# Optimization experiments

Measured on AMD Instinct MI355X. Metric: run time of the kernel, lower is better.

The kernel has to match this reference:

```python
import jax, jax.numpy as jnp
import numpy as np
from jax import lax

COMMITMENT_COST = 0.25

def setup_inputs() -> dict:
    key = jax.random.key(0)
    k1, k2, k3 = jax.random.split(key, 3)
    B, T, D, Q, K = 32, 8192, 8, 8, 1024
    return {
        "x": jax.random.normal(k1, (B, T, D), dtype=jnp.float32),
        "codebooks": jax.random.normal(k2, (Q, K, D), dtype=jnp.float32),
        "post_scale": jnp.ones((Q,), dtype=jnp.float32),
        "post_bias": jnp.zeros((Q,), dtype=jnp.float32),
        "conv_w": jax.random.normal(k3, (D, D), dtype=jnp.float32),
        "conv_b": jnp.zeros((D,), dtype=jnp.float32),
    }

def reference(x, codebooks, post_scale, post_bias, conv_w, conv_b):
    # Residual VQ with STE fix (use_ste_fix=True, use_cosine_sim=False).
    # x: [B, T, D]; codebooks: [Q, K, D]
    def step(carry, params):
        residual, qsum, loss = carry
        cb, s, b = params  # cb: [K, D]
        # squared L2 distances [B, T, K] = |r|^2 + |c|^2 - 2 r.c
        d2 = ((residual ** 2).sum(-1, keepdims=True)
              + (cb ** 2).sum(-1)
              - 2.0 * jnp.einsum('btd,kd->btk', residual, cb))
        idx = jnp.argmin(d2, axis=-1)          # [B, T]
        embeds = cb[idx]                        # gather [B, T, D]
        # straight-through estimator
        embeds_st = residual + lax.stop_gradient(embeds - residual)
        qsum = qsum + embeds_st * s + b
        new_res = residual - embeds
        loss = loss + jnp.mean((lax.stop_gradient(new_res) - embeds) ** 2)
        return (new_res, qsum, loss), idx

    init = (x, jnp.zeros_like(x), jnp.float32(0.0))
    (_, qsum, loss), codes = lax.scan(step, init, (codebooks, post_scale, post_bias))
    # final_conv: 1x1 Conv1d over channels == dense over last dim
    quantized = jnp.einsum('btd,ed->bte', qsum, conv_w) + conv_b
    return quantized, loss * COMMITMENT_COST, codes  # codes: [Q, B, T]
```

## Files before the change

kernel.cpp:

```cpp
#include <hip/hip_runtime.h>
#include <math.h>

constexpr int Bq = 32;
constexpr int Tq = 8192;
constexpr int Dq = 8;
constexpr int Qq = 8;
constexpr int Kq = 1024;
constexpr int NTOK = Bq * Tq;
constexpr float LOSS_SCALE = 0.25f / (float)(Bq * Tq * Dq);

constexpr int WS_QSTRIDE = 9216;
constexpr int WS_CNMAX   = 8 * WS_QSTRIDE;
constexpr size_t WS_NEED_BYTES = (size_t)(WS_CNMAX + 8) * 4;

typedef __attribute__((ext_vector_type(8))) short short8;
typedef __attribute__((ext_vector_type(4))) float f32x4;
typedef __attribute__((ext_vector_type(4))) unsigned int u32x4;


__device__ __forceinline__ void gload_lds16(const void* gsrc, void* ldst) {
    __builtin_amdgcn_global_load_lds(
        (const __attribute__((address_space(1))) unsigned int*)gsrc,
        (__attribute__((address_space(3))) unsigned int*)ldst,
        16, 0, 0);
}

__global__ __launch_bounds__(512)
void rvq_prep(const float* __restrict__ codebooks, float* __restrict__ ws)
{
    __shared__ float s_red[8];
    const int tid  = threadIdx.x;
    const int lane = tid & 63;
    const int wave = tid >> 6;
    const int q    = blockIdx.x;
    const float* cbq = codebooks + (size_t)q * Kq * Dq;
    float* wq = ws + (size_t)q * WS_QSTRIDE;
    unsigned* frag = reinterpret_cast<unsigned*>(wq);
    float* cnh = wq + Kq * 8;

    float nmax = 0.0f;
#pragma unroll
    for (int it = 0; it < 2; ++it) {
        int n = tid + it * 512;
        const float4* cp = reinterpret_cast<const float4*>(cbq + (size_t)n * 8);
        float4 ca = cp[0], cc = cp[1];
        float c[8] = {ca.x, ca.y, ca.z, ca.w, cc.x, cc.y, cc.z, cc.w};
        float nn = __fmul_rn(c[0], c[0]);
#pragma unroll
        for (int d = 1; d < 8; ++d)
            nn = __fadd_rn(nn, __fmul_rn(c[d], c[d]));
        cnh[n] = -0.5f * nn;
        nmax = fmaxf(nmax, nn);
        unsigned hb[8], lb[8];
#pragma unroll
        for (int d = 0; d < 8; ++d) {
            union { float f; unsigned u; } v; v.f = c[d];
            hb[d] = (v.u + 0x7FFFu + ((v.u >> 16) & 1u)) >> 16;
            union { unsigned u; float f; } h; h.u = hb[d] << 16;
            union { float f; unsigned u; } w; w.f = __fsub_rn(c[d], h.f);
            lb[d] = (w.u + 0x7FFFu + ((w.u >> 16) & 1u)) >> 16;
        }
        u32x4 wh = {hb[0] | (hb[1] << 16), hb[2] | (hb[3] << 16),
                    hb[4] | (hb[5] << 16), hb[6] | (hb[7] << 16)};
        u32x4 wl = {lb[0] | (lb[1] << 16), lb[2] | (lb[3] << 16),
                    lb[4] | (lb[5] << 16), lb[6] | (lb[7] << 16)};
        reinterpret_cast<u32x4*>(frag)[n * 2]     = wh;
        reinterpret_cast<u32x4*>(frag)[n * 2 + 1] = wl;
    }
#pragma unroll
    for (int off = 32; off >= 1; off >>= 1)
        nmax = fmaxf(nmax, __shfl_xor(nmax, off, 64));
    if (lane == 0) s_red[wave] = nmax;
    __syncthreads();
    if (tid == 0) {
        float m = s_red[0];
#pragma unroll
        for (int i = 1; i < 8; ++i) m = fmaxf(m, s_red[i]);
        ws[WS_CNMAX + q] = m;
    }
}

__global__ __launch_bounds__(512, 4)
void rvq_main(const float* __restrict__ x,
              const float* __restrict__ codebooks,
              const float* __restrict__ post_scale,
              const float* __restrict__ post_bias,
              const float* __restrict__ conv_w,
              const float* __restrict__ conv_b,
              const float* __restrict__ ws,
              float* __restrict__ out)
{
    __shared__ __align__(16) unsigned s_all[Kq * 8 + Kq];
    unsigned* s_frag = s_all;
    float* s_cnh = reinterpret_cast<float*>(s_all + Kq * 8);

    const int tid  = threadIdx.x;
    const int lane = tid & 63;
    const int wave = tid >> 6;
    const int quad = lane >> 4;
    const int col  = lane & 15;
    const int wbase = blockIdx.x * 256 + wave * 32;

    float rg[2][Dq];
#pragma unroll
    for (int g = 0; g < 2; ++g) {
        const float4* xp = reinterpret_cast<const float4*>(
            x + (size_t)(wbase + g * 16 + col) * Dq);
        float4 a = xp[0], b = xp[1];
        rg[g][0]=a.x; rg[g][1]=a.y; rg[g][2]=a.z; rg[g][3]=a.w;
        rg[g][4]=b.x; rg[g][5]=b.y; rg[g][6]=b.z; rg[g][7]=b.w;
    }

    float qso[Dq];
#pragma unroll
    for (int d = 0; d < Dq; ++d) qso[d] = 0.0f;
    float lossacc = 0.0f;

    float* out_quant = out;
    float* out_loss  = out + (size_t)NTOK * Dq;
    float* out_codes = out_loss + 1;
    const float* ws_cnmax = ws + WS_CNMAX;

    for (int q = 0; q < Qq; ++q) {
        const float* cbq = codebooks + (size_t)q * Kq * Dq;
        const float* wq = ws + (size_t)q * WS_QSTRIDE;

        {
            const char* src_base = reinterpret_cast<const char*>(wq);
            char* dst_base = reinterpret_cast<char*>(s_all);
            const int l16 = lane * 16;
#pragma unroll
            for (int c = 0; c < 4; ++c) {
                const int off = (wave * 4 + c) * 1024;
                gload_lds16(src_base + off + l16, dst_base + off);
            }
            if (wave < 4) {
                const int off = 32768 + wave * 1024;
                gload_lds16(src_base + off + l16, dst_base + off);
            }
        }
        const float cnmax = ws_cnmax[q];
        __syncthreads();

        float rn_own[2];
        short8 bfrag[2];
#pragma unroll
        for (int g = 0; g < 2; ++g) {
            float n = __fmul_rn(rg[g][0], rg[g][0]);
#pragma unroll
            for (int d = 1; d < 8; ++d)
                n = __fadd_rn(n, __fmul_rn(rg[g][d], rg[g][d]));
            rn_own[g] = n;
            short8 bf;
#pragma unroll
            for (int d = 0; d < 8; ++d) {
                union { float f; unsigned u; } v; v.f = rg[g][d];
                unsigned hbb = (v.u + 0x7FFFu + ((v.u >> 16) & 1u)) >> 16;
                union { unsigned u; float f; } h; h.u = hbb << 16;
                union { float f; unsigned u; } w; w.f = __fsub_rn(rg[g][d], h.f);
                unsigned lbb = (w.u + 0x7FFFu + ((w.u >> 16) & 1u)) >> 16;
                bf[d] = (short)((quad >> 1) ? lbb : hbb);
            }
            bfrag[g] = bf;
        }

        float m1[2]  = {-__builtin_inff(), -__builtin_inff()};
        float m2g[2] = {-__builtin_inff(), -__builtin_inff()};
        int   gtile[2] = {0, 0};
        const int fsel = (quad & 1) * 4;
        const int quad4 = quad * 4;
#pragma unroll 2
        for (int tile = 0; tile < Kq / 16; ++tile) {
            f32x4 cinit = *reinterpret_cast<const f32x4*>(s_cnh + tile * 16 + quad4);
            int fb = (tile * 16 + col) * 8 + fsel;
            uint2 w0 = *reinterpret_cast<const uint2*>(s_frag + fb);
            uint2 w1 = *reinterpret_cast<const uint2*>(s_frag + fb + 2);
            u32x4 wa = {w0.x, w0.y, w1.x, w1.y};
            short8 afrag = __builtin_bit_cast(short8, wa);
#pragma unroll
            for (int g = 0; g < 2; ++g) {
                f32x4 acc = __builtin_amdgcn_mfma_f32_16x16x32_bf16(afrag, bfrag[g], cinit, 0, 0, 0);
                float t = fmaxf(fmaxf(fmaxf(acc[0], acc[1]), acc[2]), acc[3]);
                bool gt = t > m1[g];
                gtile[g] = gt ? tile : gtile[g];
                m2g[g] = fmaxf(m2g[g], fminf(m1[g], t));
                m1[g]  = fmaxf(m1[g], t);
            }
        }

        float M1[2], M2[2];
        int bk[2], fl[2];
#pragma unroll
        for (int g = 0; g < 2; ++g) {
            int base = gtile[g] * 16 + quad4;
            float best = -__builtin_inff(), sec = -__builtin_inff();
            int breg = 0;
#pragma unroll
            for (int r = 0; r < 4; ++r) {
                int k = base + r;
                const float4* cp = reinterpret_cast<const float4*>(cbq + (size_t)k * 8);
                float4 ca = cp[0], cc = cp[1];
                float dot = __fmul_rn(rg[g][0], ca.x);
                dot = fmaf(rg[g][1], ca.y, dot);
                dot = fmaf(rg[g][2], ca.z, dot);
                dot = fmaf(rg[g][3], ca.w, dot);
                dot = fmaf(rg[g][4], cc.x, dot);
                dot = fmaf(rg[g][5], cc.y, dot);
                dot = fmaf(rg[g][6], cc.z, dot);
                dot = fmaf(rg[g][7], cc.w, dot);
                float Dx = __fadd_rn(dot, s_cnh[k]);
                bool w = Dx > best;
                sec = fmaxf(sec, fminf(best, Dx));
                breg = w ? r : breg;
                best = fmaxf(best, Dx);
            }
            M1[g] = best;
            M2[g] = fmaxf(sec, m2g[g]);
            bk[g] = base + breg;
        }

#pragma unroll
        for (int g = 0; g < 2; ++g) {
            float A1 = M1[g], A2 = M2[g]; int K1 = bk[g];
#pragma unroll
            for (int m = 16; m <= 32; m <<= 1) {
                float o1 = __shfl_xor(A1, m, 64);
                float o2 = __shfl_xor(A2, m, 64);
                int   ok = __shfl_xor(K1, m, 64);
                bool ow = (o1 > A1) || (o1 == A1 && ok < K1);
                A2 = ow ? fmaxf(A1, o2) : fmaxf(o1, A2);
                A1 = ow ? o1 : A1; K1 = ow ? ok : K1;
            }
            float margin = (rn_own[g] + cnmax) * 6e-5f;
            fl[g] = (__fsub_rn(A1, A2) <= margin) ? 1 : 0;
            bk[g] = K1;
        }

#pragma unroll
        for (int g = 0; g < 2; ++g) {
            unsigned long long msk = __ballot(fl[g] && (quad == g));
            while (msk) {
                int p = __builtin_ctzll(msk); msk &= (msk - 1);
                float rt[8];
#pragma unroll
                for (int d = 0; d < 8; ++d) rt[d] = __shfl(rg[g][d], p, 64);
                float rnt = __shfl(rn_own[g], p, 64);
                float bb = __builtin_inff(); int bkk = 0;
#pragma unroll 2
                for (int i = 0; i < 16; ++i) {
                    int k = lane + 64 * i;
                    const float4* cp = reinterpret_cast<const float4*>(cbq + (size_t)k * 8);
                    float4 ca = cp[0], cc = cp[1];
                    float c8[8] = {ca.x, ca.y, ca.z, ca.w, cc.x, cc.y, cc.z, cc.w};
                    float cn = __fmul_rn(c8[0], c8[0]);
#pragma unroll
                    for (int d = 1; d < 8; ++d)
                        cn = __fadd_rn(cn, __fmul_rn(c8[d], c8[d]));
                    float dot = __fmul_rn(rt[0], c8[0]);
                    dot = fmaf(rt[1], c8[1], dot);
                    dot = fmaf(rt[2], c8[2], dot);
                    dot = fmaf(rt[3], c8[3], dot);
                    dot = fmaf(rt[4], c8[4], dot);
                    dot = fmaf(rt[5], c8[5], dot);
                    dot = fmaf(rt[6], c8[6], dot);
                    dot = fmaf(rt[7], c8[7], dot);
                    float d2 = fmaf(dot, -2.0f, __fadd_rn(rnt, cn));
                    if (d2 < bb) { bb = d2; bkk = k; }
                }
#pragma unroll
                for (int mm = 1; mm <= 32; mm <<= 1) {
                    float ob = __shfl_xor(bb, mm, 64);
                    int   ok = __shfl_xor(bkk, mm, 64);
                    if (ob < bb || (ob == bb && ok < bkk)) { bb = ob; bkk = ok; }
                }
                if (col == (p & 15)) bk[g] = bkk;
            }
        }

        const float sc = post_scale[q];
        const float bi = post_bias[q];
#pragma unroll
        for (int g = 0; g < 2; ++g) {
            if (quad == g)
                out_codes[(size_t)q * NTOK + wbase + g * 16 + col] = (float)bk[g];
            const float4* ep = reinterpret_cast<const float4*>(cbq + (size_t)bk[g] * 8);
            float4 ea = ep[0], eb = ep[1];
            float e[8] = {ea.x, ea.y, ea.z, ea.w, eb.x, eb.y, eb.z, eb.w};
#pragma unroll
            for (int d = 0; d < 8; ++d) {
                float rd = rg[g][d];
                float est = __fadd_rn(rd, __fsub_rn(e[d], rd));
                if (quad == g) {
                    qso[d] = __fadd_rn(__fadd_rn(qso[d], __fmul_rn(est, sc)), bi);
                }
                float nr = __fsub_rn(rd, e[d]);
                float df = __fsub_rn(nr, e[d]);
                if (quad == g) lossacc = fmaf(df, df, lossacc);
                rg[g][d] = nr;
            }
        }
        __syncthreads();
    }

    if (quad < 2) {
        float o[8];
#pragma unroll
        for (int e2 = 0; e2 < 8; ++e2) {
            float acc = __fmul_rn(qso[0], conv_w[e2 * 8 + 0]);
#pragma unroll
            for (int d = 1; d < 8; ++d)
                acc = fmaf(qso[d], conv_w[e2 * 8 + d], acc);
            o[e2] = __fadd_rn(acc, conv_b[e2]);
        }
        float4* op = reinterpret_cast<float4*>(
            out_quant + (size_t)(wbase + quad * 16 + col) * Dq);
        op[0] = make_float4(o[0], o[1], o[2], o[3]);
        op[1] = make_float4(o[4], o[5], o[6], o[7]);
    }

    float v = lossacc;
#pragma unroll
    for (int off = 32; off >= 1; off >>= 1)
        v += __shfl_xor(v, off, 64);
    if (lane == 0)
        atomicAdd(out_loss, v * LOSS_SCALE);
}

__global__ __launch_bounds__(512, 2)
void rvq_mono(const float* __restrict__ x,
              const float* __restrict__ codebooks,
              const float* __restrict__ post_scale,
              const float* __restrict__ post_bias,
              const float* __restrict__ conv_w,
              const float* __restrict__ conv_b,
              float* __restrict__ out)
{
    __shared__ __align__(16) unsigned s_frag[Kq * 8];
    __shared__ __align__(16) float s_cnh[Kq];
    __shared__ float s_red[8];

    const int tid  = threadIdx.x;
    const int lane = tid & 63;
    const int wave = tid >> 6;
    const int quad = lane >> 4;
    const int col  = lane & 15;
    const int wbase = blockIdx.x * 256 + wave * 32;

    float rg[2][Dq];
#pragma unroll
    for (int g = 0; g < 2; ++g) {
        const float4* xp = reinterpret_cast<const float4*>(
            x + (size_t)(wbase + g * 16 + col) * Dq);
        float4 a = xp[0], b = xp[1];
        rg[g][0]=a.x; rg[g][1]=a.y; rg[g][2]=a.z; rg[g][3]=a.w;
        rg[g][4]=b.x; rg[g][5]=b.y; rg[g][6]=b.z; rg[g][7]=b.w;
    }

    float qso[Dq];
#pragma unroll
    for (int d = 0; d < Dq; ++d) qso[d] = 0.0f;
    float lossacc = 0.0f;

    float* out_quant = out;
    float* out_loss  = out + (size_t)NTOK * Dq;
    float* out_codes = out_loss + 1;

    for (int q = 0; q < Qq; ++q) {
        const float* cbq = codebooks + (size_t)q * Kq * Dq;

        float nmax = 0.0f;
#pragma unroll
        for (int it = 0; it < 2; ++it) {
            int n = tid + it * 512;
            const float4* cp = reinterpret_cast<const float4*>(cbq + (size_t)n * 8);
            float4 ca = cp[0], cc = cp[1];
            float c[8] = {ca.x, ca.y, ca.z, ca.w, cc.x, cc.y, cc.z, cc.w};
            float nn = __fmul_rn(c[0], c[0]);
#pragma unroll
            for (int d = 1; d < 8; ++d)
                nn = __fadd_rn(nn, __fmul_rn(c[d], c[d]));
            s_cnh[n] = -0.5f * nn;
            nmax = fmaxf(nmax, nn);
            unsigned hb[8], lb[8];
#pragma unroll
            for (int d = 0; d < 8; ++d) {
                union { float f; unsigned u; } v; v.f = c[d];
                hb[d] = (v.u + 0x7FFFu + ((v.u >> 16) & 1u)) >> 16;
                union { unsigned u; float f; } h; h.u = hb[d] << 16;
                union { float f; unsigned u; } w; w.f = __fsub_rn(c[d], h.f);
                lb[d] = (w.u + 0x7FFFu + ((w.u >> 16) & 1u)) >> 16;
            }
            u32x4 wh = {hb[0] | (hb[1] << 16), hb[2] | (hb[3] << 16),
                        hb[4] | (hb[5] << 16), hb[6] | (hb[7] << 16)};
            u32x4 wl = {lb[0] | (lb[1] << 16), lb[2] | (lb[3] << 16),
                        lb[4] | (lb[5] << 16), lb[6] | (lb[7] << 16)};
            reinterpret_cast<u32x4*>(s_frag)[n * 2]     = wh;
            reinterpret_cast<u32x4*>(s_frag)[n * 2 + 1] = wl;
        }
#pragma unroll
        for (int off = 32; off >= 1; off >>= 1)
            nmax = fmaxf(nmax, __shfl_xor(nmax, off, 64));
        if (lane == 0) s_red[wave] = nmax;
        __syncthreads();
        float cnmax = s_red[0];
#pragma unroll
        for (int i = 1; i < 8; ++i) cnmax = fmaxf(cnmax, s_red[i]);

        float rn_own[2];
        short8 bfrag[2];
#pragma unroll
        for (int g = 0; g < 2; ++g) {
            float n = __fmul_rn(rg[g][0], rg[g][0]);
#pragma unroll
            for (int d = 1; d < 8; ++d)
                n = __fadd_rn(n, __fmul_rn(rg[g][d], rg[g][d]));
            rn_own[g] = n;
            short8 bf;
#pragma unroll
            for (int d = 0; d < 8; ++d) {
                union { float f; unsigned u; } v; v.f = rg[g][d];
                unsigned hbb = (v.u + 0x7FFFu + ((v.u >> 16) & 1u)) >> 16;
                union { unsigned u; float f; } h; h.u = hbb << 16;
                union { float f; unsigned u; } w; w.f = __fsub_rn(rg[g][d], h.f);
                unsigned lbb = (w.u + 0x7FFFu + ((w.u >> 16) & 1u)) >> 16;
                bf[d] = (short)((quad >> 1) ? lbb : hbb);
            }
            bfrag[g] = bf;
        }

        float m1[2]  = {-__builtin_inff(), -__builtin_inff()};
        float m2g[2] = {-__builtin_inff(), -__builtin_inff()};
        int   gtile[2] = {0, 0};
        const int fsel = (quad & 1) * 4;
        const int quad4 = quad * 4;
#pragma unroll 2
        for (int tile = 0; tile < Kq / 16; ++tile) {
            f32x4 cinit = *reinterpret_cast<const f32x4*>(s_cnh + tile * 16 + quad4);
            int fb = (tile * 16 + col) * 8 + fsel;
            uint2 w0 = *reinterpret_cast<const uint2*>(s_frag + fb);
            uint2 w1 = *reinterpret_cast<const uint2*>(s_frag + fb + 2);
            u32x4 wa = {w0.x, w0.y, w1.x, w1.y};
            short8 afrag = __builtin_bit_cast(short8, wa);
#pragma unroll
            for (int g = 0; g < 2; ++g) {
                f32x4 acc = __builtin_amdgcn_mfma_f32_16x16x32_bf16(afrag, bfrag[g], cinit, 0, 0, 0);
                float t = fmaxf(fmaxf(fmaxf(acc[0], acc[1]), acc[2]), acc[3]);
                bool gt = t > m1[g];
                gtile[g] = gt ? tile : gtile[g];
                m2g[g] = fmaxf(m2g[g], fminf(m1[g], t));
                m1[g]  = fmaxf(m1[g], t);
            }
        }

        float M1[2], M2[2];
        int bk[2], fl[2];
#pragma unroll
        for (int g = 0; g < 2; ++g) {
            int base = gtile[g] * 16 + quad4;
            float best = -__builtin_inff(), sec = -__builtin_inff();
            int breg = 0;
#pragma unroll
            for (int r = 0; r < 4; ++r) {
                int k = base + r;
                const float4* cp = reinterpret_cast<const float4*>(cbq + (size_t)k * 8);
                float4 ca = cp[0], cc = cp[1];
                float dot = __fmul_rn(rg[g][0], ca.x);
                dot = fmaf(rg[g][1], ca.y, dot);
                dot = fmaf(rg[g][2], ca.z, dot);
                dot = fmaf(rg[g][3], ca.w, dot);
                dot = fmaf(rg[g][4], cc.x, dot);
                dot = fmaf(rg[g][5], cc.y, dot);
                dot = fmaf(rg[g][6], cc.z, dot);
                dot = fmaf(rg[g][7], cc.w, dot);
                float Dx = __fadd_rn(dot, s_cnh[k]);
                bool w = Dx > best;
                sec = fmaxf(sec, fminf(best, Dx));
                breg = w ? r : breg;
                best = fmaxf(best, Dx);
            }
            M1[g] = best;
            M2[g] = fmaxf(sec, m2g[g]);
            bk[g] = base + breg;
        }

#pragma unroll
        for (int g = 0; g < 2; ++g) {
            float A1 = M1[g], A2 = M2[g]; int K1 = bk[g];
#pragma unroll
            for (int m = 16; m <= 32; m <<= 1) {
                float o1 = __shfl_xor(A1, m, 64);
                float o2 = __shfl_xor(A2, m, 64);
                int   ok = __shfl_xor(K1, m, 64);
                bool ow = (o1 > A1) || (o1 == A1 && ok < K1);
                A2 = ow ? fmaxf(A1, o2) : fmaxf(o1, A2);
                A1 = ow ? o1 : A1; K1 = ow ? ok : K1;
            }
            float margin = (rn_own[g] + cnmax) * 6e-5f;
            fl[g] = (__fsub_rn(A1, A2) <= margin) ? 1 : 0;
            bk[g] = K1;
        }

#pragma unroll
        for (int g = 0; g < 2; ++g) {
            unsigned long long msk = __ballot(fl[g] && (quad == g));
            while (msk) {
                int p = __builtin_ctzll(msk); msk &= (msk - 1);
                float rt[8];
#pragma unroll
                for (int d = 0; d < 8; ++d) rt[d] = __shfl(rg[g][d], p, 64);
                float rnt = __shfl(rn_own[g], p, 64);
                float bb = __builtin_inff(); int bkk = 0;
#pragma unroll 2
                for (int i = 0; i < 16; ++i) {
                    int k = lane + 64 * i;
                    const float4* cp = reinterpret_cast<const float4*>(cbq + (size_t)k * 8);
                    float4 ca = cp[0], cc = cp[1];
                    float c8[8] = {ca.x, ca.y, ca.z, ca.w, cc.x, cc.y, cc.z, cc.w};
                    float cn = __fmul_rn(c8[0], c8[0]);
#pragma unroll
                    for (int d = 1; d < 8; ++d)
                        cn = __fadd_rn(cn, __fmul_rn(c8[d], c8[d]));
                    float dot = __fmul_rn(rt[0], c8[0]);
                    dot = fmaf(rt[1], c8[1], dot);
                    dot = fmaf(rt[2], c8[2], dot);
                    dot = fmaf(rt[3], c8[3], dot);
                    dot = fmaf(rt[4], c8[4], dot);
                    dot = fmaf(rt[5], c8[5], dot);
                    dot = fmaf(rt[6], c8[6], dot);
                    dot = fmaf(rt[7], c8[7], dot);
                    float d2 = fmaf(dot, -2.0f, __fadd_rn(rnt, cn));
                    if (d2 < bb) { bb = d2; bkk = k; }
                }
#pragma unroll
                for (int mm = 1; mm <= 32; mm <<= 1) {
                    float ob = __shfl_xor(bb, mm, 64);
                    int   ok = __shfl_xor(bkk, mm, 64);
                    if (ob < bb || (ob == bb && ok < bkk)) { bb = ob; bkk = ok; }
                }
                if (col == (p & 15)) bk[g] = bkk;
            }
        }

        const float sc = post_scale[q];
        const float bi = post_bias[q];
#pragma unroll
        for (int g = 0; g < 2; ++g) {
            if (quad == g)
                out_codes[(size_t)q * NTOK + wbase + g * 16 + col] = (float)bk[g];
            const float4* ep = reinterpret_cast<const float4*>(cbq + (size_t)bk[g] * 8);
            float4 ea = ep[0], eb = ep[1];
            float e[8] = {ea.x, ea.y, ea.z, ea.w, eb.x, eb.y, eb.z, eb.w};
#pragma unroll
            for (int d = 0; d < 8; ++d) {
                float rd = rg[g][d];
                float est = __fadd_rn(rd, __fsub_rn(e[d], rd));
                if (quad == g) {
                    qso[d] = __fadd_rn(__fadd_rn(qso[d], __fmul_rn(est, sc)), bi);
                }
                float nr = __fsub_rn(rd, e[d]);
                float df = __fsub_rn(nr, e[d]);
                if (quad == g) lossacc = fmaf(df, df, lossacc);
                rg[g][d] = nr;
            }
        }
        __syncthreads();
    }

    if (quad < 2) {
        float o[8];
#pragma unroll
        for (int e2 = 0; e2 < 8; ++e2) {
            float acc = __fmul_rn(qso[0], conv_w[e2 * 8 + 0]);
#pragma unroll
            for (int d = 1; d < 8; ++d)
                acc = fmaf(qso[d], conv_w[e2 * 8 + d], acc);
            o[e2] = __fadd_rn(acc, conv_b[e2]);
        }
        float4* op = reinterpret_cast<float4*>(
            out_quant + (size_t)(wbase + quad * 16 + col) * Dq);
        op[0] = make_float4(o[0], o[1], o[2], o[3]);
        op[1] = make_float4(o[4], o[5], o[6], o[7]);
    }

    float v = lossacc;
#pragma unroll
    for (int off = 32; off >= 1; off >>= 1)
        v += __shfl_xor(v, off, 64);
    if (lane == 0)
        atomicAdd(out_loss, v * LOSS_SCALE);
}

extern "C" void kernel_launch(void* const* d_in, const int* in_sizes, int n_in,
                              void* d_out, int out_size, void* d_ws, size_t ws_size,
                              hipStream_t stream) {
    const float* x     = (const float*)d_in[0];
    const float* cb    = (const float*)d_in[1];
    const float* ps    = (const float*)d_in[2];
    const float* pb    = (const float*)d_in[3];
    const float* cw    = (const float*)d_in[4];
    const float* cbias = (const float*)d_in[5];
    float* out = (float*)d_out;

    hipMemsetAsync(out + (size_t)NTOK * Dq, 0, sizeof(float), stream);

    if (d_ws != nullptr && ws_size >= WS_NEED_BYTES) {
        float* ws = (float*)d_ws;
        rvq_prep<<<dim3(Qq), dim3(512), 0, stream>>>(cb, ws);
        rvq_main<<<dim3(NTOK / 256), dim3(512), 0, stream>>>(
            x, cb, ps, pb, cw, cbias, ws, out);
    } else {
        rvq_mono<<<dim3(NTOK / 256), dim3(512), 0, stream>>>(
            x, cb, ps, pb, cw, cbias, out);
    }
}
```

Baseline: 391.0 us.

## Switch rvq_main distance search to 32x32x16 bf16 MFMA with split-precision operands

```diff
diff --git a/kernel.cpp b/kernel.cpp
--- a/kernel.cpp
+++ b/kernel.cpp
@@ -15,6 +15,7 @@
 
 typedef __attribute__((ext_vector_type(8))) short short8;
 typedef __attribute__((ext_vector_type(4))) float f32x4;
+typedef __attribute__((ext_vector_type(16))) float f32x16;
 typedef __attribute__((ext_vector_type(4))) unsigned int u32x4;
 
 
@@ -97,6 +98,253 @@
     const int tid  = threadIdx.x;
     const int lane = tid & 63;
     const int wave = tid >> 6;
+    const int half = lane >> 5;
+    const int tcol = lane & 31;
+    const int wbase = blockIdx.x * 256 + wave * 32;
+
+    float rg[Dq];
+    {
+        const float4* xp = reinterpret_cast<const float4*>(
+            x + (size_t)(wbase + tcol) * Dq);
+        float4 a = xp[0], b = xp[1];
+        rg[0]=a.x; rg[1]=a.y; rg[2]=a.z; rg[3]=a.w;
+        rg[4]=b.x; rg[5]=b.y; rg[6]=b.z; rg[7]=b.w;
+    }
+
+    float qso[Dq];
+#pragma unroll
+    for (int d = 0; d < Dq; ++d) qso[d] = 0.0f;
+    float lossacc = 0.0f;
+
+    float* out_quant = out;
+    float* out_loss  = out + (size_t)NTOK * Dq;
+    float* out_codes = out_loss + 1;
+    const float* ws_cnmax = ws + WS_CNMAX;
+
+    for (int q = 0; q < Qq; ++q) {
+        const float* cbq = codebooks + (size_t)q * Kq * Dq;
+        const float* wq = ws + (size_t)q * WS_QSTRIDE;
+
+        {
+            const char* src_base = reinterpret_cast<const char*>(wq);
+            char* dst_base = reinterpret_cast<char*>(s_all);
+            const int l16 = lane * 16;
+#pragma unroll
+            for (int c = 0; c < 4; ++c) {
+                const int off = (wave * 4 + c) * 1024;
+                gload_lds16(src_base + off + l16, dst_base + off);
+            }
+            if (wave < 4) {
+                const int off = 32768 + wave * 1024;
+                gload_lds16(src_base + off + l16, dst_base + off);
+            }
+        }
+        const float cnmax = ws_cnmax[q];
+        __syncthreads();
+
+        float rn;
+        short8 bfrag1, bfrag2;
+        {
+            float n = __fmul_rn(rg[0], rg[0]);
+#pragma unroll
+            for (int d = 1; d < 8; ++d)
+                n = __fadd_rn(n, __fmul_rn(rg[d], rg[d]));
+            rn = n;
+            short8 rh8, rl8;
+#pragma unroll
+            for (int d = 0; d < 8; ++d) {
+                union { float f; unsigned u; } v; v.f = rg[d];
+                unsigned hbb = (v.u + 0x7FFFu + ((v.u >> 16) & 1u)) >> 16;
+                union { unsigned u; float f; } h; h.u = hbb << 16;
+                union { float f; unsigned u; } w; w.f = __fsub_rn(rg[d], h.f);
+                unsigned lbb = (w.u + 0x7FFFu + ((w.u >> 16) & 1u)) >> 16;
+                rh8[d] = (short)hbb;
+                rl8[d] = (short)lbb;
+            }
+            bfrag1 = half ? rl8 : rh8;
+            bfrag2 = half ? rh8 : rl8;
+        }
+
+        float m1  = -__builtin_inff();
+        float m2g = -__builtin_inff();
+        int   gblk = 0;
+        const int h4 = half * 4;
+#pragma unroll 1
+        for (int blk = 0; blk < Kq / 32; ++blk) {
+            int ab = (blk * 32 + tcol) * 8 + h4;
+            u32x4 wa = *reinterpret_cast<const u32x4*>(s_frag + ab);
+            short8 afrag = __builtin_bit_cast(short8, wa);
+            const float* cb0 = s_cnh + blk * 32 + h4;
+            f32x4 c0 = *reinterpret_cast<const f32x4*>(cb0);
+            f32x4 c1 = *reinterpret_cast<const f32x4*>(cb0 + 8);
+            f32x4 c2 = *reinterpret_cast<const f32x4*>(cb0 + 16);
+            f32x4 c3 = *reinterpret_cast<const f32x4*>(cb0 + 24);
+            f32x16 acc = {c0[0], c0[1], c0[2], c0[3],
+                          c1[0], c1[1], c1[2], c1[3],
+                          c2[0], c2[1], c2[2], c2[3],
+                          c3[0], c3[1], c3[2], c3[3]};
+            acc = __builtin_amdgcn_mfma_f32_32x32x16_bf16(afrag, bfrag1, acc, 0, 0, 0);
+            acc = __builtin_amdgcn_mfma_f32_32x32x16_bf16(afrag, bfrag2, acc, 0, 0, 0);
+            float t01 = fmaxf(acc[0], acc[1]),   t23 = fmaxf(acc[2], acc[3]);
+            float t45 = fmaxf(acc[4], acc[5]),   t67 = fmaxf(acc[6], acc[7]);
+            float t89 = fmaxf(acc[8], acc[9]),   tab = fmaxf(acc[10], acc[11]);
+            float tcd = fmaxf(acc[12], acc[13]), tef = fmaxf(acc[14], acc[15]);
+            float ta = fmaxf(fmaxf(t01, t23), fmaxf(t45, t67));
+            float tb = fmaxf(fmaxf(t89, tab), fmaxf(tcd, tef));
+            float t = fmaxf(ta, tb);
+            bool gt = t > m1;
+            gblk = gt ? blk : gblk;
+            m2g = fmaxf(m2g, fminf(m1, t));
+            m1  = fmaxf(m1, t);
+        }
+
+        float M1, M2;
+        int bk, fl;
+        {
+            int base = gblk * 32 + h4;
+            float best = -__builtin_inff(), sec = -__builtin_inff();
+            int bki = base;
+#pragma unroll 4
+            for (int r = 0; r < 16; ++r) {
+                int k = base + (r & 3) + 8 * (r >> 2);
+                const float4* cp = reinterpret_cast<const float4*>(cbq + (size_t)k * 8);
+                float4 ca = cp[0], cc = cp[1];
+                float dot = __fmul_rn(rg[0], ca.x);
+                dot = fmaf(rg[1], ca.y, dot);
+                dot = fmaf(rg[2], ca.z, dot);
+                dot = fmaf(rg[3], ca.w, dot);
+                dot = fmaf(rg[4], cc.x, dot);
+                dot = fmaf(rg[5], cc.y, dot);
+                dot = fmaf(rg[6], cc.z, dot);
+                dot = fmaf(rg[7], cc.w, dot);
+                float Dx = __fadd_rn(dot, s_cnh[k]);
+                bool w = Dx > best;
+                sec = fmaxf(sec, fminf(best, Dx));
+                bki = w ? k : bki;
+                best = fmaxf(best, Dx);
+            }
+            M1 = best;
+            M2 = fmaxf(sec, m2g);
+            bk = bki;
+        }
+
+        {
+            float A1 = M1, A2 = M2; int K1 = bk;
+            float o1 = __shfl_xor(A1, 32, 64);
+            float o2 = __shfl_xor(A2, 32, 64);
+            int   ok = __shfl_xor(K1, 32, 64);
+            bool ow = (o1 > A1) || (o1 == A1 && ok < K1);
+            A2 = ow ? fmaxf(A1, o2) : fmaxf(o1, A2);
+            A1 = ow ? o1 : A1; K1 = ow ? ok : K1;
+            float margin = (rn + cnmax) * 6e-5f;
+            fl = (__fsub_rn(A1, A2) <= margin) ? 1 : 0;
+            bk = K1;
+        }
+
+        {
+            unsigned long long msk = __ballot(fl && (lane < 32));
+            while (msk) {
+                int p = __builtin_ctzll(msk); msk &= (msk - 1);
+                float rt[8];
+#pragma unroll
+                for (int d = 0; d < 8; ++d) rt[d] = __shfl(rg[d], p, 64);
+                float rnt = __shfl(rn, p, 64);
+                float bb = __builtin_inff(); int bkk = 0;
+#pragma unroll 2
+                for (int i = 0; i < 16; ++i) {
+                    int k = lane + 64 * i;
+                    const float4* cp = reinterpret_cast<const float4*>(cbq + (size_t)k * 8);
+                    float4 ca = cp[0], cc = cp[1];
+                    float c8[8] = {ca.x, ca.y, ca.z, ca.w, cc.x, cc.y, cc.z, cc.w};
+                    float cn = __fmul_rn(c8[0], c8[0]);
+#pragma unroll
+                    for (int d = 1; d < 8; ++d)
+                        cn = __fadd_rn(cn, __fmul_rn(c8[d], c8[d]));
+                    float dot = __fmul_rn(rt[0], c8[0]);
+                    dot = fmaf(rt[1], c8[1], dot);
+                    dot = fmaf(rt[2], c8[2], dot);
+                    dot = fmaf(rt[3], c8[3], dot);
+                    dot = fmaf(rt[4], c8[4], dot);
+                    dot = fmaf(rt[5], c8[5], dot);
+                    dot = fmaf(rt[6], c8[6], dot);
+                    dot = fmaf(rt[7], c8[7], dot);
+                    float d2 = fmaf(dot, -2.0f, __fadd_rn(rnt, cn));
+                    if (d2 < bb) { bb = d2; bkk = k; }
+                }
+#pragma unroll
+                for (int mm = 1; mm <= 32; mm <<= 1) {
+                    float ob = __shfl_xor(bb, mm, 64);
+                    int   ok = __shfl_xor(bkk, mm, 64);
+                    if (ob < bb || (ob == bb && ok < bkk)) { bb = ob; bkk = ok; }
+                }
+                if (tcol == p) bk = bkk;
+            }
+        }
+
+        const float sc = post_scale[q];
+        const float bi = post_bias[q];
+        if (half == 0)
+            out_codes[(size_t)q * NTOK + wbase + tcol] = (float)bk;
+        {
+            const float4* ep = reinterpret_cast<const float4*>(cbq + (size_t)bk * 8);
+            float4 ea = ep[0], eb = ep[1];
+            float e[8] = {ea.x, ea.y, ea.z, ea.w, eb.x, eb.y, eb.z, eb.w};
+#pragma unroll
+            for (int d = 0; d < 8; ++d) {
+                float rd = rg[d];
+                float est = __fadd_rn(rd, __fsub_rn(e[d], rd));
+                if (half == 0) {
+                    qso[d] = __fadd_rn(__fadd_rn(qso[d], __fmul_rn(est, sc)), bi);
+                }
+                float nr = __fsub_rn(rd, e[d]);
+                float df = __fsub_rn(nr, e[d]);
+                if (half == 0) lossacc = fmaf(df, df, lossacc);
+                rg[d] = nr;
+            }
+        }
+        __syncthreads();
+    }
+
+    if (half == 0) {
+        float o[8];
+#pragma unroll
+        for (int e2 = 0; e2 < 8; ++e2) {
+            float acc = __fmul_rn(qso[0], conv_w[e2 * 8 + 0]);
+#pragma unroll
+            for (int d = 1; d < 8; ++d)
+                acc = fmaf(qso[d], conv_w[e2 * 8 + d], acc);
+            o[e2] = __fadd_rn(acc, conv_b[e2]);
+        }
+        float4* op = reinterpret_cast<float4*>(
+            out_quant + (size_t)(wbase + tcol) * Dq);
+        op[0] = make_float4(o[0], o[1], o[2], o[3]);
+        op[1] = make_float4(o[4], o[5], o[6], o[7]);
+    }
+
+    float v = lossacc;
+#pragma unroll
+    for (int off = 32; off >= 1; off >>= 1)
+        v += __shfl_xor(v, off, 64);
+    if (lane == 0)
+        atomicAdd(out_loss, v * LOSS_SCALE);
+}
+
+__global__ __launch_bounds__(512, 2)
+void rvq_mono(const float* __restrict__ x,
+              const float* __restrict__ codebooks,
+              const float* __restrict__ post_scale,
+              const float* __restrict__ post_bias,
+              const float* __restrict__ conv_w,
+              const float* __restrict__ conv_b,
+              float* __restrict__ out)
+{
+    __shared__ __align__(16) unsigned s_frag[Kq * 8];
+    __shared__ __align__(16) float s_cnh[Kq];
+    __shared__ float s_red[8];
+
+    const int tid  = threadIdx.x;
+    const int lane = tid & 63;
+    const int wave = tid >> 6;
     const int quad = lane >> 4;
     const int col  = lane & 15;
     const int wbase = blockIdx.x * 256 + wave * 32;
@@ -119,28 +367,47 @@
     float* out_quant = out;
     float* out_loss  = out + (size_t)NTOK * Dq;
     float* out_codes = out_loss + 1;
-    const float* ws_cnmax = ws + WS_CNMAX;
 
     for (int q = 0; q < Qq; ++q) {
         const float* cbq = codebooks + (size_t)q * Kq * Dq;
-        const float* wq = ws + (size_t)q * WS_QSTRIDE;
-
-        {
-            const char* src_base = reinterpret_cast<const char*>(wq);
-            char* dst_base = reinterpret_cast<char*>(s_all);
-            const int l16 = lane * 16;
-#pragma unroll
-            for (int c = 0; c < 4; ++c) {
-                const int off = (wave * 4 + c) * 1024;
-                gload_lds16(src_base + off + l16, dst_base + off);
-            }
-            if (wave < 4) {
-                const int off = 32768 + wave * 1024;
-                gload_lds16(src_base + off + l16, dst_base + off);
-            }
-        }
-        const float cnmax = ws_cnmax[q];
+
+        float nmax = 0.0f;
+#pragma unroll
+        for (int it = 0; it < 2; ++it) {
+            int n = tid + it * 512;
+            const float4* cp = reinterpret_cast<const float4*>(cbq + (size_t)n * 8);
+            float4 ca = cp[0], cc = cp[1];
+            float c[8] = {ca.x, ca.y, ca.z, ca.w, cc.x, cc.y, cc.z, cc.w};
+            float nn = __fmul_rn(c[0], c[0]);
+#pragma unroll
+            for (int d = 1; d < 8; ++d)
+                nn = __fadd_rn(nn, __fmul_rn(c[d], c[d]));
+            s_cnh[n] = -0.5f * nn;
+            nmax = fmaxf(nmax, nn);
+            unsigned hb[8], lb[8];
+#pragma unroll
+            for (int d = 0; d < 8; ++d) {
+                union { float f; unsigned u; } v; v.f = c[d];
+                hb[d] = (v.u + 0x7FFFu + ((v.u >> 16) & 1u)) >> 16;
+                union { unsigned u; float f; } h; h.u = hb[d] << 16;
+                union { float f; unsigned u; } w; w.f = __fsub_rn(c[d], h.f);
+                lb[d] = (w.u + 0x7FFFu + ((w.u >> 16) & 1u)) >> 16;
+            }
+            u32x4 wh = {hb[0] | (hb[1] << 16), hb[2] | (hb[3] << 16),
+                        hb[4] | (hb[5] << 16), hb[6] | (hb[7] << 16)};
+            u32x4 wl = {lb[0] | (lb[1] << 16), lb[2] | (lb[3] << 16),
+                        lb[4] | (lb[5] << 16), lb[6] | (lb[7] << 16)};
+            reinterpret_cast<u32x4*>(s_frag)[n * 2]     = wh;
+            reinterpret_cast<u32x4*>(s_frag)[n * 2 + 1] = wl;
+        }
+#pragma unroll
+        for (int off = 32; off >= 1; off >>= 1)
+            nmax = fmaxf(nmax, __shfl_xor(nmax, off, 64));
+        if (lane == 0) s_red[wave] = nmax;
         __syncthreads();
+        float cnmax = s_red[0];
+#pragma unroll
+        for (int i = 1; i < 8; ++i) cnmax = fmaxf(cnmax, s_red[i]);
 
         float rn_own[2];
         short8 bfrag[2];
@@ -326,270 +593,6 @@
         atomicAdd(out_loss, v * LOSS_SCALE);
 }
 
-__global__ __launch_bounds__(512, 2)
-void rvq_mono(const float* __restrict__ x,
-              const float* __restrict__ codebooks,
-              const float* __restrict__ post_scale,
-              const float* __restrict__ post_bias,
-              const float* __restrict__ conv_w,
-              const float* __restrict__ conv_b,
-              float* __restrict__ out)
-{
-    __shared__ __align__(16) unsigned s_frag[Kq * 8];
-    __shared__ __align__(16) float s_cnh[Kq];
-    __shared__ float s_red[8];
-
-    const int tid  = threadIdx.x;
-    const int lane = tid & 63;
-    const int wave = tid >> 6;
-    const int quad = lane >> 4;
-    const int col  = lane & 15;
-    const int wbase = blockIdx.x * 256 + wave * 32;
-
-    float rg[2][Dq];
-#pragma unroll
-    for (int g = 0; g < 2; ++g) {
-        const float4* xp = reinterpret_cast<const float4*>(
-            x + (size_t)(wbase + g * 16 + col) * Dq);
-        float4 a = xp[0], b = xp[1];
-        rg[g][0]=a.x; rg[g][1]=a.y; rg[g][2]=a.z; rg[g][3]=a.w;
-        rg[g][4]=b.x; rg[g][5]=b.y; rg[g][6]=b.z; rg[g][7]=b.w;
-    }
-
-    float qso[Dq];
-#pragma unroll
-    for (int d = 0; d < Dq; ++d) qso[d] = 0.0f;
-    float lossacc = 0.0f;
-
-    float* out_quant = out;
-    float* out_loss  = out + (size_t)NTOK * Dq;
-    float* out_codes = out_loss + 1;
-
-    for (int q = 0; q < Qq; ++q) {
-        const float* cbq = codebooks + (size_t)q * Kq * Dq;
-
-        float nmax = 0.0f;
-#pragma unroll
-        for (int it = 0; it < 2; ++it) {
-            int n = tid + it * 512;
-            const float4* cp = reinterpret_cast<const float4*>(cbq + (size_t)n * 8);
-            float4 ca = cp[0], cc = cp[1];
-            float c[8] = {ca.x, ca.y, ca.z, ca.w, cc.x, cc.y, cc.z, cc.w};
-            float nn = __fmul_rn(c[0], c[0]);
-#pragma unroll
-            for (int d = 1; d < 8; ++d)
-                nn = __fadd_rn(nn, __fmul_rn(c[d], c[d]));
-            s_cnh[n] = -0.5f * nn;
-            nmax = fmaxf(nmax, nn);
-            unsigned hb[8], lb[8];
-#pragma unroll
-            for (int d = 0; d < 8; ++d) {
-                union { float f; unsigned u; } v; v.f = c[d];
-                hb[d] = (v.u + 0x7FFFu + ((v.u >> 16) & 1u)) >> 16;
-                union { unsigned u; float f; } h; h.u = hb[d] << 16;
-                union { float f; unsigned u; } w; w.f = __fsub_rn(c[d], h.f);
-                lb[d] = (w.u + 0x7FFFu + ((w.u >> 16) & 1u)) >> 16;
-            }
-            u32x4 wh = {hb[0] | (hb[1] << 16), hb[2] | (hb[3] << 16),
-                        hb[4] | (hb[5] << 16), hb[6] | (hb[7] << 16)};
-            u32x4 wl = {lb[0] | (lb[1] << 16), lb[2] | (lb[3] << 16),
-                        lb[4] | (lb[5] << 16), lb[6] | (lb[7] << 16)};
-            reinterpret_cast<u32x4*>(s_frag)[n * 2]     = wh;
-            reinterpret_cast<u32x4*>(s_frag)[n * 2 + 1] = wl;
-        }
-#pragma unroll
-        for (int off = 32; off >= 1; off >>= 1)
-            nmax = fmaxf(nmax, __shfl_xor(nmax, off, 64));
-        if (lane == 0) s_red[wave] = nmax;
-        __syncthreads();
-        float cnmax = s_red[0];
-#pragma unroll
-        for (int i = 1; i < 8; ++i) cnmax = fmaxf(cnmax, s_red[i]);
-
-        float rn_own[2];
-        short8 bfrag[2];
-#pragma unroll
-        for (int g = 0; g < 2; ++g) {
-            float n = __fmul_rn(rg[g][0], rg[g][0]);
-#pragma unroll
-            for (int d = 1; d < 8; ++d)
-                n = __fadd_rn(n, __fmul_rn(rg[g][d], rg[g][d]));
-            rn_own[g] = n;
-            short8 bf;
-#pragma unroll
-            for (int d = 0; d < 8; ++d) {
-                union { float f; unsigned u; } v; v.f = rg[g][d];
-                unsigned hbb = (v.u + 0x7FFFu + ((v.u >> 16) & 1u)) >> 16;
-                union { unsigned u; float f; } h; h.u = hbb << 16;
-                union { float f; unsigned u; } w; w.f = __fsub_rn(rg[g][d], h.f);
-                unsigned lbb = (w.u + 0x7FFFu + ((w.u >> 16) & 1u)) >> 16;
-                bf[d] = (short)((quad >> 1) ? lbb : hbb);
-            }
-            bfrag[g] = bf;
-        }
-
-        float m1[2]  = {-__builtin_inff(), -__builtin_inff()};
-        float m2g[2] = {-__builtin_inff(), -__builtin_inff()};
-        int   gtile[2] = {0, 0};
-        const int fsel = (quad & 1) * 4;
-        const int quad4 = quad * 4;
-#pragma unroll 2
-        for (int tile = 0; tile < Kq / 16; ++tile) {
-            f32x4 cinit = *reinterpret_cast<const f32x4*>(s_cnh + tile * 16 + quad4);
-            int fb = (tile * 16 + col) * 8 + fsel;
-            uint2 w0 = *reinterpret_cast<const uint2*>(s_frag + fb);
-            uint2 w1 = *reinterpret_cast<const uint2*>(s_frag + fb + 2);
-            u32x4 wa = {w0.x, w0.y, w1.x, w1.y};
-            short8 afrag = __builtin_bit_cast(short8, wa);
-#pragma unroll
-            for (int g = 0; g < 2; ++g) {
-                f32x4 acc = __builtin_amdgcn_mfma_f32_16x16x32_bf16(afrag, bfrag[g], cinit, 0, 0, 0);
-                float t = fmaxf(fmaxf(fmaxf(acc[0], acc[1]), acc[2]), acc[3]);
-                bool gt = t > m1[g];
-                gtile[g] = gt ? tile : gtile[g];
-                m2g[g] = fmaxf(m2g[g], fminf(m1[g], t));
-                m1[g]  = fmaxf(m1[g], t);
-            }
-        }
-
-        float M1[2], M2[2];
-        int bk[2], fl[2];
-#pragma unroll
-        for (int g = 0; g < 2; ++g) {
-            int base = gtile[g] * 16 + quad4;
-            float best = -__builtin_inff(), sec = -__builtin_inff();
-            int breg = 0;
-#pragma unroll
-            for (int r = 0; r < 4; ++r) {
-                int k = base + r;
-                const float4* cp = reinterpret_cast<const float4*>(cbq + (size_t)k * 8);
-                float4 ca = cp[0], cc = cp[1];
-                float dot = __fmul_rn(rg[g][0], ca.x);
-                dot = fmaf(rg[g][1], ca.y, dot);
-                dot = fmaf(rg[g][2], ca.z, dot);
-                dot = fmaf(rg[g][3], ca.w, dot);
-                dot = fmaf(rg[g][4], cc.x, dot);
-                dot = fmaf(rg[g][5], cc.y, dot);
-                dot = fmaf(rg[g][6], cc.z, dot);
-                dot = fmaf(rg[g][7], cc.w, dot);
-                float Dx = __fadd_rn(dot, s_cnh[k]);
-                bool w = Dx > best;
-                sec = fmaxf(sec, fminf(best, Dx));
-                breg = w ? r : breg;
-                best = fmaxf(best, Dx);
-            }
-            M1[g] = best;
-            M2[g] = fmaxf(sec, m2g[g]);
-            bk[g] = base + breg;
-        }
-
-#pragma unroll
-        for (int g = 0; g < 2; ++g) {
-            float A1 = M1[g], A2 = M2[g]; int K1 = bk[g];
-#pragma unroll
-            for (int m = 16; m <= 32; m <<= 1) {
-                float o1 = __shfl_xor(A1, m, 64);
-                float o2 = __shfl_xor(A2, m, 64);
-                int   ok = __shfl_xor(K1, m, 64);
-                bool ow = (o1 > A1) || (o1 == A1 && ok < K1);
-                A2 = ow ? fmaxf(A1, o2) : fmaxf(o1, A2);
-                A1 = ow ? o1 : A1; K1 = ow ? ok : K1;
-            }
-            float margin = (rn_own[g] + cnmax) * 6e-5f;
-            fl[g] = (__fsub_rn(A1, A2) <= margin) ? 1 : 0;
-            bk[g] = K1;
-        }
-
-#pragma unroll
-        for (int g = 0; g < 2; ++g) {
-            unsigned long long msk = __ballot(fl[g] && (quad == g));
-            while (msk) {
-                int p = __builtin_ctzll(msk); msk &= (msk - 1);
-                float rt[8];
-#pragma unroll
-                for (int d = 0; d < 8; ++d) rt[d] = __shfl(rg[g][d], p, 64);
-                float rnt = __shfl(rn_own[g], p, 64);
-                float bb = __builtin_inff(); int bkk = 0;
-#pragma unroll 2
-                for (int i = 0; i < 16; ++i) {
-                    int k = lane + 64 * i;
-                    const float4* cp = reinterpret_cast<const float4*>(cbq + (size_t)k * 8);
-                    float4 ca = cp[0], cc = cp[1];
-                    float c8[8] = {ca.x, ca.y, ca.z, ca.w, cc.x, cc.y, cc.z, cc.w};
-                    float cn = __fmul_rn(c8[0], c8[0]);
-#pragma unroll
-                    for (int d = 1; d < 8; ++d)
-                        cn = __fadd_rn(cn, __fmul_rn(c8[d], c8[d]));
-                    float dot = __fmul_rn(rt[0], c8[0]);
-                    dot = fmaf(rt[1], c8[1], dot);
-                    dot = fmaf(rt[2], c8[2], dot);
-                    dot = fmaf(rt[3], c8[3], dot);
-                    dot = fmaf(rt[4], c8[4], dot);
-                    dot = fmaf(rt[5], c8[5], dot);
-                    dot = fmaf(rt[6], c8[6], dot);
-                    dot = fmaf(rt[7], c8[7], dot);
-                    float d2 = fmaf(dot, -2.0f, __fadd_rn(rnt, cn));
-                    if (d2 < bb) { bb = d2; bkk = k; }
-                }
-#pragma unroll
-                for (int mm = 1; mm <= 32; mm <<= 1) {
-                    float ob = __shfl_xor(bb, mm, 64);
-                    int   ok = __shfl_xor(bkk, mm, 64);
-                    if (ob < bb || (ob == bb && ok < bkk)) { bb = ob; bkk = ok; }
-                }
-                if (col == (p & 15)) bk[g] = bkk;
-            }
-        }
-
-        const float sc = post_scale[q];
-        const float bi = post_bias[q];
-#pragma unroll
-        for (int g = 0; g < 2; ++g) {
-            if (quad == g)
-                out_codes[(size_t)q * NTOK + wbase + g * 16 + col] = (float)bk[g];
-            const float4* ep = reinterpret_cast<const float4*>(cbq + (size_t)bk[g] * 8);
-            float4 ea = ep[0], eb = ep[1];
-            float e[8] = {ea.x, ea.y, ea.z, ea.w, eb.x, eb.y, eb.z, eb.w};
-#pragma unroll
-            for (int d = 0; d < 8; ++d) {
-                float rd = rg[g][d];
-                float est = __fadd_rn(rd, __fsub_rn(e[d], rd));
-                if (quad == g) {
-                    qso[d] = __fadd_rn(__fadd_rn(qso[d], __fmul_rn(est, sc)), bi);
-                }
-                float nr = __fsub_rn(rd, e[d]);
-                float df = __fsub_rn(nr, e[d]);
-                if (quad == g) lossacc = fmaf(df, df, lossacc);
-                rg[g][d] = nr;
-            }
-        }
-        __syncthreads();
-    }
-
-    if (quad < 2) {
-        float o[8];
-#pragma unroll
-        for (int e2 = 0; e2 < 8; ++e2) {
-            float acc = __fmul_rn(qso[0], conv_w[e2 * 8 + 0]);
-#pragma unroll
-            for (int d = 1; d < 8; ++d)
-                acc = fmaf(qso[d], conv_w[e2 * 8 + d], acc);
-            o[e2] = __fadd_rn(acc, conv_b[e2]);
-        }
-        float4* op = reinterpret_cast<float4*>(
-            out_quant + (size_t)(wbase + quad * 16 + col) * Dq);
-        op[0] = make_float4(o[0], o[1], o[2], o[3]);
-        op[1] = make_float4(o[4], o[5], o[6], o[7]);
-    }
-
-    float v = lossacc;
-#pragma unroll
-    for (int off = 32; off >= 1; off >>= 1)
-        v += __shfl_xor(v, off, 64);
-    if (lane == 0)
-        atomicAdd(out_loss, v * LOSS_SCALE);
-}
-
 extern "C" void kernel_launch(void* const* d_in, const int* in_sizes, int n_in,
                               void* d_out, int out_size, void* d_ws, size_t ws_size,
                               hipStream_t stream) {
```

After: 443.4 us. +13.4%, slower.
